# Kernel optimization log

Hardware: AMD Instinct MI355X
Metric: run time of the kernel (lower is better)

Reference implementation:

```python
import jax, jax.numpy as jnp
import numpy as np

B, S, D, H, DFF = 2, 2048, 512, 8, 2048
DK = D // H
EPS = 1e-6  # LayerNormalization eps


def _ln(x, a, b):
    # torch: alpha * (x - mean) / (std + eps) + bias, std is unbiased (ddof=1)
    m = jnp.mean(x, axis=-1, keepdims=True)
    s = jnp.std(x, axis=-1, keepdims=True, ddof=1)
    return a * (x - m) / (s + EPS) + b


def _mha(Q, K, V, mask, Wq, bq, Wk, bk, Wv, bv, Wo, bo):
    Bq, Sq = Q.shape[0], Q.shape[1]
    Sk = K.shape[1]
    q = (Q @ Wq + bq).reshape(Bq, Sq, H, DK).transpose(0, 2, 1, 3)  # bhqd
    k = (K @ Wk + bk).reshape(Bq, Sk, H, DK).transpose(0, 2, 1, 3)  # bhkd
    v = (V @ Wv + bv).reshape(Bq, Sk, H, DK).transpose(0, 2, 1, 3)  # bhkd
    scores = jnp.einsum('bhqd,bhkd->bhqk', q, k) / jnp.sqrt(jnp.float32(DK))
    scores = jnp.where(mask == 0, -jnp.inf, scores)  # masked_fill(mask==0, -inf)
    attn = jax.nn.softmax(scores, axis=-1)  # dropout is identity in eval
    out = jnp.einsum('bhqk,bhkd->bhqd', attn, v)
    out = out.transpose(0, 2, 1, 3).reshape(Bq, Sq, D)
    return out @ Wo + bo


def setup_inputs() -> dict:
    key = jax.random.key(0)
    ks = jax.random.split(key, 20)
    sc = 0.02
    inp = {
        'x': jax.random.normal(ks[0], (B, S, D), jnp.float32),
        'encoder_output': jax.random.normal(ks[1], (B, S, D), jnp.float32),
        'encoder_output_mask': jnp.broadcast_to(jnp.ones((S, S), jnp.int32), (B, 1, S, S)),
        'decoder_mask': jnp.broadcast_to(jnp.tril(jnp.ones((S, S), jnp.int32)), (B, 1, S, S)),
        'sa_Wq': jax.random.normal(ks[2], (D, D), jnp.float32) * sc,
        'sa_bq': jnp.zeros((D,), jnp.float32),
        'sa_Wk': jax.random.normal(ks[3], (D, D), jnp.float32) * sc,
        'sa_bk': jnp.zeros((D,), jnp.float32),
        'sa_Wv': jax.random.normal(ks[4], (D, D), jnp.float32) * sc,
        'sa_bv': jnp.zeros((D,), jnp.float32),
        'sa_Wo': jax.random.normal(ks[5], (D, D), jnp.float32) * sc,
        'sa_bo': jnp.zeros((D,), jnp.float32),
        'ca_Wq': jax.random.normal(ks[6], (D, D), jnp.float32) * sc,
        'ca_bq': jnp.zeros((D,), jnp.float32),
        'ca_Wk': jax.random.normal(ks[7], (D, D), jnp.float32) * sc,
        'ca_bk': jnp.zeros((D,), jnp.float32),
        'ca_Wv': jax.random.normal(ks[8], (D, D), jnp.float32) * sc,
        'ca_bv': jnp.zeros((D,), jnp.float32),
        'ca_Wo': jax.random.normal(ks[9], (D, D), jnp.float32) * sc,
        'ca_bo': jnp.zeros((D,), jnp.float32),
        'ff_W1': jax.random.normal(ks[10], (D, DFF), jnp.float32) * sc,
        'ff_b1': jnp.zeros((DFF,), jnp.float32),
        'ff_W2': jax.random.normal(ks[11], (DFF, D), jnp.float32) * sc,
        'ff_b2': jnp.zeros((D,), jnp.float32),
        'ln0_a': jnp.ones((1,), jnp.float32), 'ln0_b': jnp.zeros((1,), jnp.float32),
        'ln1_a': jnp.ones((1,), jnp.float32), 'ln1_b': jnp.zeros((1,), jnp.float32),
        'ln2_a': jnp.ones((1,), jnp.float32), 'ln2_b': jnp.zeros((1,), jnp.float32),
    }
    return inp


def reference(x, encoder_output, encoder_output_mask, decoder_mask,
              sa_Wq, sa_bq, sa_Wk, sa_bk, sa_Wv, sa_bv, sa_Wo, sa_bo,
              ca_Wq, ca_bq, ca_Wk, ca_bk, ca_Wv, ca_bv, ca_Wo, ca_bo,
              ff_W1, ff_b1, ff_W2, ff_b2,
              ln0_a, ln0_b, ln1_a, ln1_b, ln2_a, ln2_b):
    # Residual 0: pre-norm self-attention (dropout = identity in eval)
    n = _ln(x, ln0_a, ln0_b)
    x = x + _mha(n, n, n, decoder_mask, sa_Wq, sa_bq, sa_Wk, sa_bk, sa_Wv, sa_bv, sa_Wo, sa_bo)
    # Residual 1: pre-norm cross-attention
    n = _ln(x, ln1_a, ln1_b)
    x = x + _mha(n, encoder_output, encoder_output, encoder_output_mask,
                 ca_Wq, ca_bq, ca_Wk, ca_bk, ca_Wv, ca_bv, ca_Wo, ca_bo)
    # Residual 2: pre-norm FFN (Linear -> ReLU -> Linear)
    n = _ln(x, ln2_a, ln2_b)
    x = x + (jax.nn.relu(n @ ff_W1 + ff_b1) @ ff_W2 + ff_b2)
    return x
```

## Files before the change

kernel.cpp:

```cpp
#include <hip/hip_runtime.h>
#include <hip/hip_bf16.h>

typedef __bf16 bf16_t;
typedef __bf16 bf16x8_t __attribute__((ext_vector_type(8)));
typedef float f32x4_t __attribute__((ext_vector_type(4)));

static constexpr int B_ = 2, S_ = 2048, D_ = 512, H_ = 8, DK_ = 64, DFF_ = 2048;
static constexpr int M_ = B_ * S_;
static constexpr float QSCALE = 0.125f * 1.44269504f;

#define VMCNT_BARRIER(N) asm volatile("s_waitcnt vmcnt(" #N ")\n\ts_barrier" ::: "memory")

__device__ __forceinline__ unsigned pkbf(float a, float b) {
  union { bf16_t h; unsigned short u; } x, y;
  x.h = (bf16_t)a; y.h = (bf16_t)b;
  return (unsigned)x.u | ((unsigned)y.u << 16);
}

__device__ __forceinline__ void async16(bf16_t* lds, const bf16_t* g) {
  __builtin_amdgcn_global_load_lds((__attribute__((address_space(1))) void*)g,
                                   (__attribute__((address_space(3))) void*)lds,
                                   16, 0, 0);
}

__global__ __launch_bounds__(256) void ln_kernel(const float* __restrict__ x,
                                                 const float* __restrict__ ga,
                                                 const float* __restrict__ gb,
                                                 bf16_t* __restrict__ out) {
  const int row = blockIdx.x * 4 + (threadIdx.x >> 6);
  const int lane = threadIdx.x & 63;
  const float4* xr = (const float4*)(x + (long)row * D_);
  float4 v0 = xr[lane * 2];
  float4 v1 = xr[lane * 2 + 1];
  float s = v0.x + v0.y + v0.z + v0.w + v1.x + v1.y + v1.z + v1.w;
  float ss = v0.x * v0.x + v0.y * v0.y + v0.z * v0.z + v0.w * v0.w +
             v1.x * v1.x + v1.y * v1.y + v1.z * v1.z + v1.w * v1.w;
#pragma unroll
  for (int m = 1; m < 64; m <<= 1) {
    s += __shfl_xor(s, m);
    ss += __shfl_xor(ss, m);
  }
  const float mean = s * (1.0f / 512.0f);
  float var = (ss - 512.0f * mean * mean) * (1.0f / 511.0f);
  var = fmaxf(var, 0.0f);
  const float sc = ga[0] / (sqrtf(var) + 1e-6f);
  const float sh = gb[0] - mean * sc;
  alignas(16) bf16_t y[8];
  y[0] = (bf16_t)(v0.x * sc + sh);
  y[1] = (bf16_t)(v0.y * sc + sh);
  y[2] = (bf16_t)(v0.z * sc + sh);
  y[3] = (bf16_t)(v0.w * sc + sh);
  y[4] = (bf16_t)(v1.x * sc + sh);
  y[5] = (bf16_t)(v1.y * sc + sh);
  y[6] = (bf16_t)(v1.z * sc + sh);
  y[7] = (bf16_t)(v1.w * sc + sh);
  ((uint4*)(out + (long)row * D_))[lane] = *(uint4*)y;
}

__global__ __launch_bounds__(256) void cvt_bf16(const float* __restrict__ x,
                                                bf16_t* __restrict__ y) {
  const long i = ((long)blockIdx.x * 256 + threadIdx.x) * 8;
  float4 a = *(const float4*)(x + i);
  float4 b = *(const float4*)(x + i + 4);
  alignas(16) bf16_t t[8];
  t[0] = (bf16_t)a.x; t[1] = (bf16_t)a.y; t[2] = (bf16_t)a.z; t[3] = (bf16_t)a.w;
  t[4] = (bf16_t)b.x; t[5] = (bf16_t)b.y; t[6] = (bf16_t)b.z; t[7] = (bf16_t)b.w;
  *(uint4*)(y + i) = *(uint4*)t;
}

__device__ __forceinline__ void wtrans_body(const float* __restrict__ W,
                                            bf16_t* __restrict__ Wt, int K, int N,
                                            int k0, int n0) {
  constexpr int LDT = 65;
  __shared__ float T[64 * LDT];
  const int tid = threadIdx.x;
#pragma unroll
  for (int p = 0; p < 4; ++p) {
    int e = p * 1024 + tid * 4;
    int kr = e >> 6, nc = e & 63;
    float4 f = *(const float4*)(W + (long)(k0 + kr) * N + n0 + nc);
    T[kr * LDT + nc + 0] = f.x;
    T[kr * LDT + nc + 1] = f.y;
    T[kr * LDT + nc + 2] = f.z;
    T[kr * LDT + nc + 3] = f.w;
  }
  __syncthreads();
#pragma unroll
  for (int p = 0; p < 4; ++p) {
    int e = p * 1024 + tid * 4;
    int nr = e >> 6, kc = e & 63;
    alignas(8) bf16_t t[4];
#pragma unroll
    for (int j = 0; j < 4; ++j) t[j] = (bf16_t)T[(kc + j) * LDT + nr];
    *(uint2*)(Wt + (long)(n0 + nr) * K + k0 + kc) = *(uint2*)t;
  }
}

struct WPA { const float* W[10]; bf16_t* T[10]; };
__global__ __launch_bounds__(256) void wprep(WPA a) {
  const int x = blockIdx.x;
  if (x < 512) {
    const int wi = x >> 6, t = x & 63;
    wtrans_body(a.W[wi], a.T[wi], 512, 512, (t >> 3) * 64, (t & 7) * 64);
  } else if (x < 768) {
    const int t = x - 512;
    wtrans_body(a.W[8], a.T[8], 512, 2048, (t & 7) * 64, (t >> 3) * 64);
  } else {
    const int t = x - 768;
    wtrans_body(a.W[9], a.T[9], 2048, 512, (t & 31) * 64, (t >> 5) * 64);
  }
}

__global__ __launch_bounds__(256) void vtrans(const bf16_t* __restrict__ v,
                                              bf16_t* __restrict__ vt) {
  constexpr int LDT = 66;
  __shared__ bf16_t T[64 * LDT];
  const int tid = threadIdx.x;
  const int bh = blockIdx.y, b = bh >> 3, h = bh & 7;
  const int s0 = blockIdx.x * 64;
#pragma unroll
  for (int p = 0; p < 2; ++p) {
    int e = p * 2048 + tid * 8;
    int sr = e >> 6, c = e & 63;
    uint4 u = *(const uint4*)(v + (long)(b * S_ + s0 + sr) * D_ + h * DK_ + c);
    bf16_t* pv = (bf16_t*)&u;
#pragma unroll
    for (int j = 0; j < 8; ++j) T[(c + j) * LDT + sr] = pv[j];
  }
  __syncthreads();
#pragma unroll
  for (int p = 0; p < 2; ++p) {
    int e = p * 2048 + tid * 8;
    int d = e >> 6, sc = e & 63;
    alignas(16) bf16_t t[8];
#pragma unroll
    for (int j = 0; j < 8; ++j) t[j] = T[d * LDT + sc + j];
    *(uint4*)(vt + ((long)bh * DK_ + d) * S_ + s0 + sc) = *(uint4*)t;
  }
}

struct GArg {
  const bf16_t* A;
  const bf16_t* Wt;
  const float* bias;
  const float* res;
  void* out;
  float oscale;
};

template <int MODE>
__global__ __launch_bounds__(256, 2) void gemm_bt(GArg g0, GArg g1, GArg g2,
                                                  int M, int N, int K) {
  __shared__ bf16_t As[3][64 * 64];
  __shared__ bf16_t Bs[3][128 * 64];
  GArg g = (blockIdx.z == 0) ? g0 : (blockIdx.z == 1) ? g1 : g2;
  const int tid = threadIdx.x;
  const int wave = tid >> 6, lane = tid & 63, quad = lane >> 4, l15 = lane & 15;
  const long m0 = (long)blockIdx.x * 64;
  const long n0 = (long)blockIdx.y * 128;
  const int wm = (wave >> 1) * 32;
  const int wn = (wave & 1) * 64;

  const int r8 = lane >> 3;
  const int cg = (lane & 7) ^ r8;
  const bf16_t* Ab = g.A + m0 * (long)K + cg * 8;
  const bf16_t* Bb = g.Wt + n0 * (long)K + cg * 8;

  auto stage = [&](int buf, int k0) {
#pragma unroll
    for (int c = 0; c < 2; ++c) {
      const int row = wave * 16 + c * 8;
      async16(&As[buf][row * 64], Ab + (long)(row + r8) * K + k0);
    }
#pragma unroll
    for (int c = 0; c < 4; ++c) {
      const int row = wave * 32 + c * 8;
      async16(&Bs[buf][row * 64], Bb + (long)(row + r8) * K + k0);
    }
  };

  f32x4_t acc[2][4];
#pragma unroll
  for (int i = 0; i < 2; ++i)
#pragma unroll
    for (int j = 0; j < 4; ++j) acc[i][j] = (f32x4_t){0.f, 0.f, 0.f, 0.f};

  const int KT = K >> 6;
  stage(0, 0);
  stage(1, 64);
  int bc = 0;
  for (int kt = 0; kt < KT; ++kt) {
    if (kt + 1 < KT) { VMCNT_BARRIER(6); } else { VMCNT_BARRIER(0); }
    int bs = bc + 2; if (bs >= 3) bs -= 3;
    if (kt + 2 < KT) stage(bs, (kt + 2) * 64);
    const bf16_t* Al = &As[bc][0];
    const bf16_t* Bl = &Bs[bc][0];
    bf16x8_t af[2][2], bfr[2][4];
#pragma unroll
    for (int ks = 0; ks < 2; ++ks) {
      const int sc = ((ks * 4 + quad) ^ (l15 & 7)) * 8;
#pragma unroll
      for (int i = 0; i < 2; ++i)
        af[ks][i] = *(const bf16x8_t*)&Al[(wm + i * 16 + l15) * 64 + sc];
#pragma unroll
      for (int j = 0; j < 4; ++j)
        bfr[ks][j] = *(const bf16x8_t*)&Bl[(wn + j * 16 + l15) * 64 + sc];
    }
#pragma unroll
    for (int ks = 0; ks < 2; ++ks)
#pragma unroll
      for (int i = 0; i < 2; ++i)
#pragma unroll
        for (int j = 0; j < 4; ++j)
          acc[i][j] = __builtin_amdgcn_mfma_f32_16x16x32_bf16(af[ks][i], bfr[ks][j], acc[i][j], 0, 0, 0);
    bc = (bc + 1 == 3) ? 0 : bc + 1;
  }

#pragma unroll
  for (int i = 0; i < 2; ++i) {
#pragma unroll
    for (int j = 0; j < 4; ++j) {
      const long col = n0 + wn + j * 16 + l15;
      const float bv = g.bias[col];
#pragma unroll
      for (int r = 0; r < 4; ++r) {
        const long row = m0 + wm + i * 16 + quad * 4 + r;
        float v = acc[i][j][r] + bv;
        if constexpr (MODE == 1) v = fmaxf(v, 0.f);
        if constexpr (MODE == 2) {
          ((float*)g.out)[row * N + col] = v + g.res[row * N + col];
        } else {
          ((bf16_t*)g.out)[row * N + col] = (bf16_t)(v * g.oscale);
        }
      }
    }
  }
}

template <bool CAUSAL>
__global__ __launch_bounds__(256, 2) void flash_attn(const bf16_t* __restrict__ Q,
                                                     const bf16_t* __restrict__ Kg,
                                                     const bf16_t* __restrict__ Vt,
                                                     float* __restrict__ po,
                                                     float* __restrict__ pl) {
  __shared__ bf16_t Ks[3][64 * 64];
  __shared__ bf16_t Vs[3][64 * 64];
  __shared__ bf16_t Ps[4][32 * 64];
  const int tid = threadIdx.x, wave = tid >> 6, lane = tid & 63;
  const int quad = lane >> 4, l15 = lane & 15;
  const int bh = blockIdx.y, b = bh >> 3, h = bh & 7;
  const int qt = CAUSAL ? (15 - (int)blockIdx.x) : (int)blockIdx.x;
  const int chunk = blockIdx.z;
  const int ntt = CAUSAL ? (2 * qt + 2) : 32;
  const int n0t = ntt >> 1;
  const int tstart = chunk ? n0t : 0;
  const int tend = chunk ? ntt : n0t;

  const int q0 = qt * 128;
  const int qw = q0 + wave * 32;
  const long base = (long)b * S_ * D_ + (long)h * DK_;
  const long vtbase = (long)bh * DK_ * S_;
  const long prow0 = ((long)(chunk * 16 + bh)) * 2048;

  bf16x8_t qf[2][2];
#pragma unroll
  for (int qh = 0; qh < 2; ++qh)
#pragma unroll
    for (int ks = 0; ks < 2; ++ks)
      qf[qh][ks] = *(const bf16x8_t*)(Q + base + (long)(qw + qh * 16 + l15) * D_ + ks * 32 + quad * 8);

  const int r8 = lane >> 3;
  const int cg8 = (lane & 7) ^ r8;
  const bf16_t* Kb = Kg + base + cg8 * 8;
  const bf16_t* Vb = Vt + vtbase + cg8 * 8;

  auto stage = [&](int buf, int t) {
    const int kk0 = t * 64;
#pragma unroll
    for (int c = 0; c < 2; ++c) {
      const int row = wave * 16 + c * 8;
      async16(&Ks[buf][row * 64], Kb + (long)(kk0 + row + r8) * D_);
      async16(&Vs[buf][row * 64], Vb + (long)(row + r8) * S_ + kk0);
    }
  };

  float li[2] = {0.f, 0.f};
  f32x4_t o[2][4];
#pragma unroll
  for (int qh = 0; qh < 2; ++qh)
#pragma unroll
    for (int db = 0; db < 4; ++db) o[qh][db] = (f32x4_t){0.f, 0.f, 0.f, 0.f};

  bf16_t* Pw = &Ps[wave][0];
  const int pq7 = l15 & 7;

  stage(0, tstart);
  if (tstart + 1 < tend) stage(1, tstart + 1);
  int bc = 0;
  for (int t = tstart; t < tend; ++t) {
    if (t + 1 < tend) { VMCNT_BARRIER(4); } else { VMCNT_BARRIER(0); }
    int bs = bc + 2; if (bs >= 3) bs -= 3;
    if (t + 2 < tend) stage(bs, t + 2);
    const bf16_t* Kt = &Ks[bc][0];
    const bf16_t* Vl = &Vs[bc][0];
    const int kk0 = t * 64;

#pragma unroll
    for (int qh = 0; qh < 2; ++qh) {
      f32x4_t st[4];
#pragma unroll
      for (int nb = 0; nb < 4; ++nb) {
        f32x4_t a = (f32x4_t){0.f, 0.f, 0.f, 0.f};
#pragma unroll
        for (int ks = 0; ks < 2; ++ks) {
          const int scf = ((ks * 4 + quad) ^ (l15 & 7)) * 8;
          const bf16x8_t kf = *(const bf16x8_t*)&Kt[(nb * 16 + l15) * 64 + scf];
          a = __builtin_amdgcn_mfma_f32_16x16x32_bf16(kf, qf[qh][ks], a, 0, 0, 0);
        }
        st[nb] = a;
      }
      const bool domask = CAUSAL && (kk0 + 63 > qw + qh * 16);
#pragma unroll
      for (int nb = 0; nb < 4; ++nb)
#pragma unroll
        for (int r = 0; r < 4; ++r) {
          float v = st[nb][r];
          if (domask && (kk0 + nb * 16 + quad * 4 + r > qw + qh * 16 + l15)) v = -1e30f;
          const float p = exp2f(v);
          st[nb][r] = p;
          li[qh] += p;
        }
      const int prow = (qh * 16 + l15) * 64;
#pragma unroll
      for (int nb = 0; nb < 4; ++nb) {
        uint2 w;
        w.x = pkbf(st[nb][0], st[nb][1]);
        w.y = pkbf(st[nb][2], st[nb][3]);
        const int ck = nb * 2 + (quad >> 1);
        *(uint2*)&Pw[prow + (ck ^ pq7) * 8 + (quad & 1) * 4] = w;
      }
    }

    bf16x8_t pf[2][2];
#pragma unroll
    for (int qh = 0; qh < 2; ++qh)
#pragma unroll
      for (int ks = 0; ks < 2; ++ks)
        pf[qh][ks] = *(const bf16x8_t*)&Pw[(qh * 16 + l15) * 64 + (((ks * 4 + quad) ^ pq7)) * 8];
#pragma unroll
    for (int ks = 0; ks < 2; ++ks) {
#pragma unroll
      for (int db = 0; db < 4; ++db) {
        const int scf = ((ks * 4 + quad) ^ (l15 & 7)) * 8;
        const bf16x8_t vf = *(const bf16x8_t*)&Vl[(db * 16 + l15) * 64 + scf];
#pragma unroll
        for (int qh = 0; qh < 2; ++qh)
          o[qh][db] = __builtin_amdgcn_mfma_f32_16x16x32_bf16(vf, pf[qh][ks], o[qh][db], 0, 0, 0);
      }
    }
    bc = (bc + 1 == 3) ? 0 : bc + 1;
  }

#pragma unroll
  for (int qh = 0; qh < 2; ++qh) {
    li[qh] += __shfl_xor(li[qh], 16);
    li[qh] += __shfl_xor(li[qh], 32);
    const long pr = prow0 + qw + qh * 16 + l15;
#pragma unroll
    for (int db = 0; db < 4; ++db)
      *(f32x4_t*)&po[pr * 64 + db * 16 + quad * 4] = o[qh][db];
    if (quad == 0) pl[pr] = li[qh];
  }
}

__global__ __launch_bounds__(256) void merge_attn(const float* __restrict__ po,
                                                  const float* __restrict__ pl,
                                                  bf16_t* __restrict__ O) {
  const int qt = blockIdx.x, bh = blockIdx.y, b = bh >> 3, h = bh & 7;
  const int t = threadIdx.x;
  const int q = qt * 64 + (t >> 2), d0 = (t & 3) * 16;
  const long r0 = (long)bh * 2048 + q;
  const long r1 = (long)(16 + bh) * 2048 + q;
  const float inv = 1.0f / (pl[r0] + pl[r1]);
  const long i0 = r0 * 64 + d0;
  const long i1 = r1 * 64 + d0;
  alignas(16) bf16_t out[16];
#pragma unroll
  for (int j = 0; j < 4; ++j) {
    f32x4_t a = *(const f32x4_t*)&po[i0 + j * 4];
    f32x4_t c = *(const f32x4_t*)&po[i1 + j * 4];
#pragma unroll
    for (int r = 0; r < 4; ++r) out[j * 4 + r] = (bf16_t)((a[r] + c[r]) * inv);
  }
  const long row = (long)b * S_ + q;
  *(uint4*)(O + row * D_ + h * DK_ + d0) = *(uint4*)&out[0];
  *(uint4*)(O + row * D_ + h * DK_ + d0 + 8) = *(uint4*)&out[8];
}

extern "C" void kernel_launch(void* const* d_in, const int* in_sizes, int n_in,
                              void* d_out, int out_size, void* d_ws, size_t ws_size,
                              hipStream_t stream) {
  const float* x    = (const float*)d_in[0];
  const float* enc  = (const float*)d_in[1];
  const float* saWq = (const float*)d_in[4];  const float* sabq = (const float*)d_in[5];
  const float* saWk = (const float*)d_in[6];  const float* sabk = (const float*)d_in[7];
  const float* saWv = (const float*)d_in[8];  const float* sabv = (const float*)d_in[9];
  const float* saWo = (const float*)d_in[10]; const float* sabo = (const float*)d_in[11];
  const float* caWq = (const float*)d_in[12]; const float* cabq = (const float*)d_in[13];
  const float* caWk = (const float*)d_in[14]; const float* cabk = (const float*)d_in[15];
  const float* caWv = (const float*)d_in[16]; const float* cabv = (const float*)d_in[17];
  const float* caWo = (const float*)d_in[18]; const float* cabo = (const float*)d_in[19];
  const float* ffW1 = (const float*)d_in[20]; const float* ffb1 = (const float*)d_in[21];
  const float* ffW2 = (const float*)d_in[22]; const float* ffb2 = (const float*)d_in[23];
  const float* ln0a = (const float*)d_in[24]; const float* ln0b = (const float*)d_in[25];
  const float* ln1a = (const float*)d_in[26]; const float* ln1b = (const float*)d_in[27];
  const float* ln2a = (const float*)d_in[28]; const float* ln2b = (const float*)d_in[29];

  char* ws = (char*)d_ws;
  size_t off = 0;
  auto alloc = [&](size_t bytes) -> void* {
    void* p = ws + off;
    off += (bytes + 255) & ~(size_t)255;
    return p;
  };
  bf16_t* wt_saq = (bf16_t*)alloc(512 * 512 * 2);
  bf16_t* wt_sak = (bf16_t*)alloc(512 * 512 * 2);
  bf16_t* wt_sav = (bf16_t*)alloc(512 * 512 * 2);
  bf16_t* wt_sao = (bf16_t*)alloc(512 * 512 * 2);
  bf16_t* wt_caq = (bf16_t*)alloc(512 * 512 * 2);
  bf16_t* wt_cak = (bf16_t*)alloc(512 * 512 * 2);
  bf16_t* wt_cav = (bf16_t*)alloc(512 * 512 * 2);
  bf16_t* wt_cao = (bf16_t*)alloc(512 * 512 * 2);
  bf16_t* wt_f1  = (bf16_t*)alloc((size_t)512 * 2048 * 2);
  bf16_t* wt_f2  = (bf16_t*)alloc((size_t)2048 * 512 * 2);
  bf16_t* enc_b  = (bf16_t*)alloc((size_t)M_ * D_ * 2);
  bf16_t* nbuf   = (bf16_t*)alloc((size_t)M_ * D_ * 2);
  bf16_t* qb     = (bf16_t*)alloc((size_t)M_ * D_ * 2);
  bf16_t* kb     = (bf16_t*)alloc((size_t)M_ * D_ * 2);
  bf16_t* vb     = (bf16_t*)alloc((size_t)M_ * D_ * 2);
  bf16_t* vtb    = (bf16_t*)alloc((size_t)M_ * D_ * 2);
  bf16_t* attnb  = (bf16_t*)alloc((size_t)M_ * D_ * 2);
  bf16_t* hid    = (bf16_t*)alloc((size_t)M_ * DFF_ * 2);
  float*  x1     = (float*)alloc((size_t)M_ * D_ * 4);
  float*  x2     = (float*)alloc((size_t)M_ * D_ * 4);
  float*  pl     = (float*)alloc(2 * 16 * 2048 * 4);
  float*  po     = (float*)hid;

  {
    WPA a;
    a.W[0] = saWq; a.T[0] = wt_saq;
    a.W[1] = saWk; a.T[1] = wt_sak;
    a.W[2] = saWv; a.T[2] = wt_sav;
    a.W[3] = saWo; a.T[3] = wt_sao;
    a.W[4] = caWq; a.T[4] = wt_caq;
    a.W[5] = caWk; a.T[5] = wt_cak;
    a.W[6] = caWv; a.T[6] = wt_cav;
    a.W[7] = caWo; a.T[7] = wt_cao;
    a.W[8] = ffW1; a.T[8] = wt_f1;
    a.W[9] = ffW2; a.T[9] = wt_f2;
    wprep<<<1024, 256, 0, stream>>>(a);
  }
  cvt_bf16<<<1024, 256, 0, stream>>>(enc, enc_b);

  ln_kernel<<<1024, 256, 0, stream>>>(x, ln0a, ln0b, nbuf);
  {
    GArg z0{nbuf, wt_saq, sabq, nullptr, qb, QSCALE};
    GArg z1{nbuf, wt_sak, sabk, nullptr, kb, 1.0f};
    GArg z2{nbuf, wt_sav, sabv, nullptr, vb, 1.0f};
    gemm_bt<0><<<dim3(64, 4, 3), 256, 0, stream>>>(z0, z1, z2, M_, 512, 512);
  }
  vtrans<<<dim3(32, 16), 256, 0, stream>>>(vb, vtb);
  flash_attn<true><<<dim3(16, 16, 2), 256, 0, stream>>>(qb, kb, vtb, po, pl);
  merge_attn<<<dim3(32, 16), 256, 0, stream>>>(po, pl, attnb);
  {
    GArg o1{attnb, wt_sao, sabo, x, x1, 1.0f};
    gemm_bt<2><<<dim3(64, 4, 1), 256, 0, stream>>>(o1, o1, o1, M_, 512, 512);
  }

  ln_kernel<<<1024, 256, 0, stream>>>(x1, ln1a, ln1b, nbuf);
  {
    GArg c0{nbuf,  wt_caq, cabq, nullptr, qb, QSCALE};
    GArg c1{enc_b, wt_cak, cabk, nullptr, kb, 1.0f};
    GArg c2{enc_b, wt_cav, cabv, nullptr, vb, 1.0f};
    gemm_bt<0><<<dim3(64, 4, 3), 256, 0, stream>>>(c0, c1, c2, M_, 512, 512);
  }
  vtrans<<<dim3(32, 16), 256, 0, stream>>>(vb, vtb);
  flash_attn<false><<<dim3(16, 16, 2), 256, 0, stream>>>(qb, kb, vtb, po, pl);
  merge_attn<<<dim3(32, 16), 256, 0, stream>>>(po, pl, attnb);
  {
    GArg o2{attnb, wt_cao, cabo, x1, x2, 1.0f};
    gemm_bt<2><<<dim3(64, 4, 1), 256, 0, stream>>>(o2, o2, o2, M_, 512, 512);
  }

  ln_kernel<<<1024, 256, 0, stream>>>(x2, ln2a, ln2b, nbuf);
  {
    GArg f1{nbuf, wt_f1, ffb1, nullptr, hid, 1.0f};
    gemm_bt<1><<<dim3(64, 16, 1), 256, 0, stream>>>(f1, f1, f1, M_, DFF_, 512);
  }
  {
    GArg f2{hid, wt_f2, ffb2, x2, d_out, 1.0f};
    gemm_bt<2><<<dim3(64, 4, 1), 256, 0, stream>>>(f2, f2, f2, M_, 512, DFF_);
  }
}
```

Measured before the change: 385.9 us.

## Fold LayerNorm into GEMM epilogues, merge prep kernels, fuse V transpose, split attention three ways

LayerNorm is applied algebraically inside the projection GEMM epilogues. The GEMMs read an unnormalized bf16 copy of the input and correct with per-row stats and weight column sums, so the separate LN kernels go away. The residual GEMMs emit bf16 copies and accumulate row sum and sum-of-squares with atomics. Weight prep, encoder conversion, stats and column sums are merged into one prep kernel. The V transpose is fused into the QKV GEMM store, the projection GEMMs move to 128x128 tiles with K=32 double buffering, and flash attention is split into three KV chunks. Risks are extra bf16 rounding error from normalizing after the matmul and atomic accumulation order.

```diff
diff --git a/kernel.cpp b/kernel.cpp
--- a/kernel.cpp
+++ b/kernel.cpp
@@ -8,8 +8,6 @@
 static constexpr int B_ = 2, S_ = 2048, D_ = 512, H_ = 8, DK_ = 64, DFF_ = 2048;
 static constexpr int M_ = B_ * S_;
 static constexpr float QSCALE = 0.125f * 1.44269504f;
-
-#define VMCNT_BARRIER(N) asm volatile("s_waitcnt vmcnt(" #N ")\n\ts_barrier" ::: "memory")
 
 __device__ __forceinline__ unsigned pkbf(float a, float b) {
   union { bf16_t h; unsigned short u; } x, y;
@@ -23,137 +21,221 @@
                                    16, 0, 0);
 }
 
-__global__ __launch_bounds__(256) void ln_kernel(const float* __restrict__ x,
-                                                 const float* __restrict__ ga,
-                                                 const float* __restrict__ gb,
-                                                 bf16_t* __restrict__ out) {
-  const int row = blockIdx.x * 4 + (threadIdx.x >> 6);
-  const int lane = threadIdx.x & 63;
-  const float4* xr = (const float4*)(x + (long)row * D_);
-  float4 v0 = xr[lane * 2];
-  float4 v1 = xr[lane * 2 + 1];
-  float s = v0.x + v0.y + v0.z + v0.w + v1.x + v1.y + v1.z + v1.w;
-  float ss = v0.x * v0.x + v0.y * v0.y + v0.z * v0.z + v0.w * v0.w +
-             v1.x * v1.x + v1.y * v1.y + v1.z * v1.z + v1.w * v1.w;
-#pragma unroll
-  for (int m = 1; m < 64; m <<= 1) {
-    s += __shfl_xor(s, m);
-    ss += __shfl_xor(ss, m);
-  }
-  const float mean = s * (1.0f / 512.0f);
-  float var = (ss - 512.0f * mean * mean) * (1.0f / 511.0f);
+struct PrepArg {
+  const float* W[10]; bf16_t* T[10];
+  const float* enc; bf16_t* encb;
+  const float* x; bf16_t* xb; float2* stats0;
+  float* stats12;
+  float* csum[7];
+};
+
+__global__ __launch_bounds__(256) void prep(PrepArg a) {
+  __shared__ float T[64 * 65];
+  const int bx = blockIdx.x, tid = threadIdx.x;
+  if (bx < 1024) {
+    const float* W; bf16_t* Wt; int K, N, k0, n0;
+    if (bx < 512) { int wi = bx >> 6, t = bx & 63; W = a.W[wi]; Wt = a.T[wi]; K = 512; N = 512; k0 = (t >> 3) * 64; n0 = (t & 7) * 64; }
+    else if (bx < 768) { int t = bx - 512; W = a.W[8]; Wt = a.T[8]; K = 512; N = 2048; k0 = (t & 7) * 64; n0 = (t >> 3) * 64; }
+    else { int t = bx - 768; W = a.W[9]; Wt = a.T[9]; K = 2048; N = 512; k0 = (t & 31) * 64; n0 = (t >> 5) * 64; }
+#pragma unroll
+    for (int p = 0; p < 4; ++p) {
+      int e = p * 1024 + tid * 4;
+      int kr = e >> 6, nc = e & 63;
+      float4 f = *(const float4*)(W + (long)(k0 + kr) * N + n0 + nc);
+      T[kr * 65 + nc + 0] = f.x; T[kr * 65 + nc + 1] = f.y;
+      T[kr * 65 + nc + 2] = f.z; T[kr * 65 + nc + 3] = f.w;
+    }
+    __syncthreads();
+#pragma unroll
+    for (int p = 0; p < 4; ++p) {
+      int e = p * 1024 + tid * 4;
+      int nr = e >> 6, kc = e & 63;
+      alignas(8) bf16_t t4[4];
+#pragma unroll
+      for (int j = 0; j < 4; ++j) t4[j] = (bf16_t)T[(kc + j) * 65 + nr];
+      *(uint2*)(Wt + (long)(n0 + nr) * K + k0 + kc) = *(uint2*)t4;
+    }
+  } else if (bx < 2048) {
+    const long i = ((long)(bx - 1024) * 256 + tid) * 8;
+    float4 u = *(const float4*)(a.enc + i);
+    float4 v = *(const float4*)(a.enc + i + 4);
+    alignas(16) bf16_t t[8];
+    t[0] = (bf16_t)u.x; t[1] = (bf16_t)u.y; t[2] = (bf16_t)u.z; t[3] = (bf16_t)u.w;
+    t[4] = (bf16_t)v.x; t[5] = (bf16_t)v.y; t[6] = (bf16_t)v.z; t[7] = (bf16_t)v.w;
+    *(uint4*)(a.encb + i) = *(uint4*)t;
+  } else if (bx < 3072) {
+    const int row = (bx - 2048) * 4 + (tid >> 6);
+    const int lane = tid & 63;
+    const float4* xr = (const float4*)(a.x + (long)row * D_);
+    float4 v0 = xr[lane * 2], v1 = xr[lane * 2 + 1];
+    float s = v0.x + v0.y + v0.z + v0.w + v1.x + v1.y + v1.z + v1.w;
+    float ss = v0.x * v0.x + v0.y * v0.y + v0.z * v0.z + v0.w * v0.w +
+               v1.x * v1.x + v1.y * v1.y + v1.z * v1.z + v1.w * v1.w;
+#pragma unroll
+    for (int m = 1; m < 64; m <<= 1) { s += __shfl_xor(s, m); ss += __shfl_xor(ss, m); }
+    alignas(16) bf16_t y[8];
+    y[0] = (bf16_t)v0.x; y[1] = (bf16_t)v0.y; y[2] = (bf16_t)v0.z; y[3] = (bf16_t)v0.w;
+    y[4] = (bf16_t)v1.x; y[5] = (bf16_t)v1.y; y[6] = (bf16_t)v1.z; y[7] = (bf16_t)v1.w;
+    ((uint4*)(a.xb + (long)row * D_))[lane] = *(uint4*)y;
+    if (lane == 0) a.stats0[row] = make_float2(s, ss);
+  } else if (bx < 3152) {
+    __shared__ float red[256];
+    int b3 = bx - 3072;
+    const float* Wsrc; float* dst; int N, c0;
+    if (b3 < 48) {
+      const int map[6] = {0, 1, 2, 4, 5, 6};
+      int wsel = b3 >> 3;
+      Wsrc = a.W[map[wsel]]; dst = a.csum[wsel]; N = 512; c0 = (b3 & 7) * 64;
+    } else { Wsrc = a.W[8]; dst = a.csum[6]; N = 2048; c0 = (b3 - 48) * 64; }
+    const int col = c0 + (tid & 63);
+    float p = 0.f;
+    for (int k = tid >> 6; k < 512; k += 4) p += Wsrc[(long)k * N + col];
+    red[tid] = p;
+    __syncthreads();
+    if (tid < 64) dst[c0 + tid] = red[tid] + red[tid + 64] + red[tid + 128] + red[tid + 192];
+  } else {
+    const int i = (bx - 3152) * 2048 + tid * 8;
+    *(f32x4_t*)&a.stats12[i] = (f32x4_t){0.f, 0.f, 0.f, 0.f};
+    *(f32x4_t*)&a.stats12[i + 4] = (f32x4_t){0.f, 0.f, 0.f, 0.f};
+  }
+}
+
+__device__ __forceinline__ void ln_coef(float2 st, float ga, float gb,
+                                        float& sc, float& sh) {
+  const float mean = st.x * (1.0f / 512.0f);
+  float var = (st.y - 512.0f * mean * mean) * (1.0f / 511.0f);
   var = fmaxf(var, 0.0f);
-  const float sc = ga[0] / (sqrtf(var) + 1e-6f);
-  const float sh = gb[0] - mean * sc;
-  alignas(16) bf16_t y[8];
-  y[0] = (bf16_t)(v0.x * sc + sh);
-  y[1] = (bf16_t)(v0.y * sc + sh);
-  y[2] = (bf16_t)(v0.z * sc + sh);
-  y[3] = (bf16_t)(v0.w * sc + sh);
-  y[4] = (bf16_t)(v1.x * sc + sh);
-  y[5] = (bf16_t)(v1.y * sc + sh);
-  y[6] = (bf16_t)(v1.z * sc + sh);
-  y[7] = (bf16_t)(v1.w * sc + sh);
-  ((uint4*)(out + (long)row * D_))[lane] = *(uint4*)y;
-}
-
-__global__ __launch_bounds__(256) void cvt_bf16(const float* __restrict__ x,
-                                                bf16_t* __restrict__ y) {
-  const long i = ((long)blockIdx.x * 256 + threadIdx.x) * 8;
-  float4 a = *(const float4*)(x + i);
-  float4 b = *(const float4*)(x + i + 4);
-  alignas(16) bf16_t t[8];
-  t[0] = (bf16_t)a.x; t[1] = (bf16_t)a.y; t[2] = (bf16_t)a.z; t[3] = (bf16_t)a.w;
-  t[4] = (bf16_t)b.x; t[5] = (bf16_t)b.y; t[6] = (bf16_t)b.z; t[7] = (bf16_t)b.w;
-  *(uint4*)(y + i) = *(uint4*)t;
-}
-
-__device__ __forceinline__ void wtrans_body(const float* __restrict__ W,
-                                            bf16_t* __restrict__ Wt, int K, int N,
-                                            int k0, int n0) {
-  constexpr int LDT = 65;
-  __shared__ float T[64 * LDT];
+  sc = ga / (sqrtf(var) + 1e-6f);
+  sh = gb - mean * sc;
+}
+
+struct G128 {
+  const bf16_t* A[3]; const bf16_t* Wt[3];
+  const float* bias[3]; const float* csum[3];
+  void* out[3]; float osc[3];
+  const float2* stats; const float* ga; const float* gb;
+  int N; int zvt;
+};
+
+template <int RELU>
+__global__ __launch_bounds__(256, 2) void gemm128(G128 a) {
+  __shared__ bf16_t As[2][128 * 32];
+  __shared__ bf16_t Bs[2][128 * 32];
+  const int z = blockIdx.z;
+  const bf16_t* A = a.A[z];
+  const bf16_t* Wt = a.Wt[z];
+  const float* bias = a.bias[z];
+  const float* csum = a.csum[z];
+  const int N = a.N;
   const int tid = threadIdx.x;
-#pragma unroll
-  for (int p = 0; p < 4; ++p) {
-    int e = p * 1024 + tid * 4;
-    int kr = e >> 6, nc = e & 63;
-    float4 f = *(const float4*)(W + (long)(k0 + kr) * N + n0 + nc);
-    T[kr * LDT + nc + 0] = f.x;
-    T[kr * LDT + nc + 1] = f.y;
-    T[kr * LDT + nc + 2] = f.z;
-    T[kr * LDT + nc + 3] = f.w;
-  }
-  __syncthreads();
-#pragma unroll
-  for (int p = 0; p < 4; ++p) {
-    int e = p * 1024 + tid * 4;
-    int nr = e >> 6, kc = e & 63;
-    alignas(8) bf16_t t[4];
-#pragma unroll
-    for (int j = 0; j < 4; ++j) t[j] = (bf16_t)T[(kc + j) * LDT + nr];
-    *(uint2*)(Wt + (long)(n0 + nr) * K + k0 + kc) = *(uint2*)t;
-  }
-}
-
-struct WPA { const float* W[10]; bf16_t* T[10]; };
-__global__ __launch_bounds__(256) void wprep(WPA a) {
-  const int x = blockIdx.x;
-  if (x < 512) {
-    const int wi = x >> 6, t = x & 63;
-    wtrans_body(a.W[wi], a.T[wi], 512, 512, (t >> 3) * 64, (t & 7) * 64);
-  } else if (x < 768) {
-    const int t = x - 512;
-    wtrans_body(a.W[8], a.T[8], 512, 2048, (t & 7) * 64, (t >> 3) * 64);
+  const int wave = tid >> 6, lane = tid & 63, quad = lane >> 4, l15 = lane & 15;
+  const long m0 = (long)blockIdx.x * 128;
+  const long n0 = (long)blockIdx.y * 128;
+  const int wm = (wave >> 1) * 64;
+  const int wn = (wave & 1) * 64;
+
+  const int r4 = lane >> 2;
+  const int cg = (lane & 3) ^ ((lane >> 3) & 3);
+  const bf16_t* Ab = A + m0 * 512 + cg * 8;
+  const bf16_t* Bb = Wt + n0 * 512 + cg * 8;
+
+  auto stage = [&](int buf, int k0) {
+#pragma unroll
+    for (int c = 0; c < 2; ++c) {
+      const int row = wave * 32 + c * 16;
+      async16(&As[buf][row * 32], Ab + (long)(row + r4) * 512 + k0);
+      async16(&Bs[buf][row * 32], Bb + (long)(row + r4) * 512 + k0);
+    }
+  };
+
+  f32x4_t acc[4][4];
+#pragma unroll
+  for (int i = 0; i < 4; ++i)
+#pragma unroll
+    for (int j = 0; j < 4; ++j) acc[i][j] = (f32x4_t){0.f, 0.f, 0.f, 0.f};
+
+  const int sc8 = (quad ^ ((l15 >> 1) & 3)) * 8;
+  stage(0, 0);
+  for (int kt = 0; kt < 16; ++kt) {
+    __syncthreads();
+    if (kt + 1 < 16) stage((kt + 1) & 1, (kt + 1) * 32);
+    const bf16_t* Al = &As[kt & 1][0];
+    const bf16_t* Bl = &Bs[kt & 1][0];
+    bf16x8_t af[4], bfr[4];
+#pragma unroll
+    for (int i = 0; i < 4; ++i) af[i] = *(const bf16x8_t*)&Al[(wm + i * 16 + l15) * 32 + sc8];
+#pragma unroll
+    for (int j = 0; j < 4; ++j) bfr[j] = *(const bf16x8_t*)&Bl[(wn + j * 16 + l15) * 32 + sc8];
+#pragma unroll
+    for (int i = 0; i < 4; ++i)
+#pragma unroll
+      for (int j = 0; j < 4; ++j)
+        acc[i][j] = __builtin_amdgcn_mfma_f32_16x16x32_bf16(af[i], bfr[j], acc[i][j], 0, 0, 0);
+  }
+
+  const bool useln = (csum != nullptr);
+  float scr[4][4], shr[4][4];
+  if (useln) {
+    const float gav = a.ga[0], gbv = a.gb[0];
+#pragma unroll
+    for (int i = 0; i < 4; ++i)
+#pragma unroll
+      for (int r = 0; r < 4; ++r) {
+        const int row = (int)m0 + wm + i * 16 + quad * 4 + r;
+        ln_coef(a.stats[row], gav, gbv, scr[i][r], shr[i][r]);
+      }
   } else {
-    const int t = x - 768;
-    wtrans_body(a.W[9], a.T[9], 2048, 512, (t & 31) * 64, (t >> 5) * 64);
-  }
-}
-
-__global__ __launch_bounds__(256) void vtrans(const bf16_t* __restrict__ v,
-                                              bf16_t* __restrict__ vt) {
-  constexpr int LDT = 66;
-  __shared__ bf16_t T[64 * LDT];
-  const int tid = threadIdx.x;
-  const int bh = blockIdx.y, b = bh >> 3, h = bh & 7;
-  const int s0 = blockIdx.x * 64;
-#pragma unroll
-  for (int p = 0; p < 2; ++p) {
-    int e = p * 2048 + tid * 8;
-    int sr = e >> 6, c = e & 63;
-    uint4 u = *(const uint4*)(v + (long)(b * S_ + s0 + sr) * D_ + h * DK_ + c);
-    bf16_t* pv = (bf16_t*)&u;
-#pragma unroll
-    for (int j = 0; j < 8; ++j) T[(c + j) * LDT + sr] = pv[j];
-  }
-  __syncthreads();
-#pragma unroll
-  for (int p = 0; p < 2; ++p) {
-    int e = p * 2048 + tid * 8;
-    int d = e >> 6, sc = e & 63;
-    alignas(16) bf16_t t[8];
-#pragma unroll
-    for (int j = 0; j < 8; ++j) t[j] = T[d * LDT + sc + j];
-    *(uint4*)(vt + ((long)bh * DK_ + d) * S_ + s0 + sc) = *(uint4*)t;
-  }
-}
-
-struct GArg {
-  const bf16_t* A;
-  const bf16_t* Wt;
-  const float* bias;
-  const float* res;
-  void* out;
-  float oscale;
-};
-
-template <int MODE>
-__global__ __launch_bounds__(256, 2) void gemm_bt(GArg g0, GArg g1, GArg g2,
-                                                  int M, int N, int K) {
-  __shared__ bf16_t As[3][64 * 64];
-  __shared__ bf16_t Bs[3][128 * 64];
-  GArg g = (blockIdx.z == 0) ? g0 : (blockIdx.z == 1) ? g1 : g2;
+#pragma unroll
+    for (int i = 0; i < 4; ++i)
+#pragma unroll
+      for (int r = 0; r < 4; ++r) { scr[i][r] = 1.f; shr[i][r] = 0.f; }
+  }
+
+  const bool isVt = (z == a.zvt);
+  const float osc = a.osc[z];
+#pragma unroll
+  for (int i = 0; i < 4; ++i) {
+#pragma unroll
+    for (int j = 0; j < 4; ++j) {
+      const int col = (int)n0 + wn + j * 16 + l15;
+      const float cs = useln ? csum[col] : 0.f;
+      const float bv = bias[col];
+      float v[4];
+#pragma unroll
+      for (int r = 0; r < 4; ++r) {
+        v[r] = scr[i][r] * acc[i][j][r] + shr[i][r] * cs + bv;
+        if constexpr (RELU == 1) v[r] = fmaxf(v[r], 0.f);
+      }
+      if (isVt) {
+        const int row0 = (int)m0 + wm + i * 16 + quad * 4;
+        const int b = row0 >> 11, s = row0 & 2047;
+        const long addr = ((long)(b * 8 + (col >> 6)) * 64 + (col & 63)) * 2048 + s;
+        uint2 w;
+        w.x = pkbf(v[0], v[1]);
+        w.y = pkbf(v[2], v[3]);
+        *(uint2*)((bf16_t*)a.out[z] + addr) = w;
+      } else {
+        bf16_t* outp = (bf16_t*)a.out[z];
+#pragma unroll
+        for (int r = 0; r < 4; ++r) {
+          const long row = m0 + wm + i * 16 + quad * 4 + r;
+          outp[row * N + col] = (bf16_t)(v[r] * osc);
+        }
+      }
+    }
+  }
+}
+
+template <bool STATS>
+__global__ __launch_bounds__(256, 3) void gemm64(const bf16_t* __restrict__ A, int K,
+                                                 const bf16_t* __restrict__ Wt,
+                                                 const float* __restrict__ bias,
+                                                 const float* __restrict__ res,
+                                                 float* __restrict__ out,
+                                                 bf16_t* __restrict__ outb,
+                                                 float* __restrict__ statsOut) {
+  __shared__ bf16_t As[2][64 * 64];
+  __shared__ bf16_t Bs[2][128 * 64];
   const int tid = threadIdx.x;
   const int wave = tid >> 6, lane = tid & 63, quad = lane >> 4, l15 = lane & 15;
   const long m0 = (long)blockIdx.x * 64;
@@ -163,8 +245,8 @@
 
   const int r8 = lane >> 3;
   const int cg = (lane & 7) ^ r8;
-  const bf16_t* Ab = g.A + m0 * (long)K + cg * 8;
-  const bf16_t* Bb = g.Wt + n0 * (long)K + cg * 8;
+  const bf16_t* Ab = A + m0 * (long)K + cg * 8;
+  const bf16_t* Bb = Wt + n0 * (long)K + cg * 8;
 
   auto stage = [&](int buf, int k0) {
 #pragma unroll
@@ -187,64 +269,72 @@
 
   const int KT = K >> 6;
   stage(0, 0);
-  stage(1, 64);
-  int bc = 0;
   for (int kt = 0; kt < KT; ++kt) {
-    if (kt + 1 < KT) { VMCNT_BARRIER(6); } else { VMCNT_BARRIER(0); }
-    int bs = bc + 2; if (bs >= 3) bs -= 3;
-    if (kt + 2 < KT) stage(bs, (kt + 2) * 64);
-    const bf16_t* Al = &As[bc][0];
-    const bf16_t* Bl = &Bs[bc][0];
-    bf16x8_t af[2][2], bfr[2][4];
+    __syncthreads();
+    if (kt + 1 < KT) stage((kt + 1) & 1, (kt + 1) * 64);
+    const bf16_t* Al = &As[kt & 1][0];
+    const bf16_t* Bl = &Bs[kt & 1][0];
 #pragma unroll
     for (int ks = 0; ks < 2; ++ks) {
       const int sc = ((ks * 4 + quad) ^ (l15 & 7)) * 8;
+      bf16x8_t af[2], bfr[4];
+#pragma unroll
+      for (int i = 0; i < 2; ++i) af[i] = *(const bf16x8_t*)&Al[(wm + i * 16 + l15) * 64 + sc];
+#pragma unroll
+      for (int j = 0; j < 4; ++j) bfr[j] = *(const bf16x8_t*)&Bl[(wn + j * 16 + l15) * 64 + sc];
 #pragma unroll
       for (int i = 0; i < 2; ++i)
-        af[ks][i] = *(const bf16x8_t*)&Al[(wm + i * 16 + l15) * 64 + sc];
-#pragma unroll
-      for (int j = 0; j < 4; ++j)
-        bfr[ks][j] = *(const bf16x8_t*)&Bl[(wn + j * 16 + l15) * 64 + sc];
-    }
-#pragma unroll
-    for (int ks = 0; ks < 2; ++ks)
-#pragma unroll
-      for (int i = 0; i < 2; ++i)
 #pragma unroll
         for (int j = 0; j < 4; ++j)
-          acc[i][j] = __builtin_amdgcn_mfma_f32_16x16x32_bf16(af[ks][i], bfr[ks][j], acc[i][j], 0, 0, 0);
-    bc = (bc + 1 == 3) ? 0 : bc + 1;
+          acc[i][j] = __builtin_amdgcn_mfma_f32_16x16x32_bf16(af[i], bfr[j], acc[i][j], 0, 0, 0);
+    }
   }
 
 #pragma unroll
   for (int i = 0; i < 2; ++i) {
+    float rs[4] = {0.f, 0.f, 0.f, 0.f}, rq[4] = {0.f, 0.f, 0.f, 0.f};
 #pragma unroll
     for (int j = 0; j < 4; ++j) {
-      const long col = n0 + wn + j * 16 + l15;
-      const float bv = g.bias[col];
+      const int col = (int)n0 + wn + j * 16 + l15;
+      const float bv = bias[col];
 #pragma unroll
       for (int r = 0; r < 4; ++r) {
         const long row = m0 + wm + i * 16 + quad * 4 + r;
-        float v = acc[i][j][r] + bv;
-        if constexpr (MODE == 1) v = fmaxf(v, 0.f);
-        if constexpr (MODE == 2) {
-          ((float*)g.out)[row * N + col] = v + g.res[row * N + col];
-        } else {
-          ((bf16_t*)g.out)[row * N + col] = (bf16_t)(v * g.oscale);
+        const float v = acc[i][j][r] + bv + res[row * 512 + col];
+        out[row * 512 + col] = v;
+        if constexpr (STATS) {
+          outb[row * 512 + col] = (bf16_t)v;
+          rs[r] += v;
+          rq[r] += v * v;
         }
       }
     }
+    if constexpr (STATS) {
+#pragma unroll
+      for (int r = 0; r < 4; ++r) {
+#pragma unroll
+        for (int m = 1; m < 16; m <<= 1) {
+          rs[r] += __shfl_xor(rs[r], m);
+          rq[r] += __shfl_xor(rq[r], m);
+        }
+        if (l15 == 0) {
+          const long row = m0 + wm + i * 16 + quad * 4 + r;
+          atomicAdd(&statsOut[row * 2], rs[r]);
+          atomicAdd(&statsOut[row * 2 + 1], rq[r]);
+        }
+      }
+    }
   }
 }
 
 template <bool CAUSAL>
-__global__ __launch_bounds__(256, 2) void flash_attn(const bf16_t* __restrict__ Q,
+__global__ __launch_bounds__(256, 3) void flash_attn(const bf16_t* __restrict__ Q,
                                                      const bf16_t* __restrict__ Kg,
                                                      const bf16_t* __restrict__ Vt,
                                                      float* __restrict__ po,
                                                      float* __restrict__ pl) {
-  __shared__ bf16_t Ks[3][64 * 64];
-  __shared__ bf16_t Vs[3][64 * 64];
+  __shared__ bf16_t Ks[2][64 * 64];
+  __shared__ bf16_t Vs[2][64 * 64];
   __shared__ bf16_t Ps[4][32 * 64];
   const int tid = threadIdx.x, wave = tid >> 6, lane = tid & 63;
   const int quad = lane >> 4, l15 = lane & 15;
@@ -252,15 +342,23 @@
   const int qt = CAUSAL ? (15 - (int)blockIdx.x) : (int)blockIdx.x;
   const int chunk = blockIdx.z;
   const int ntt = CAUSAL ? (2 * qt + 2) : 32;
-  const int n0t = ntt >> 1;
-  const int tstart = chunk ? n0t : 0;
-  const int tend = chunk ? ntt : n0t;
-
+  const int tstart = (chunk * ntt) / 3;
+  const int tend = ((chunk + 1) * ntt) / 3;
   const int q0 = qt * 128;
+  const long prow0 = ((long)(chunk * 16 + bh)) * 2048;
+
+  if (tstart >= tend) {
+    const long ob = (prow0 + q0) * 64;
+#pragma unroll
+    for (int p = 0; p < 8; ++p)
+      *(f32x4_t*)&po[ob + (long)tid * 32 + p * 4] = (f32x4_t){0.f, 0.f, 0.f, 0.f};
+    if (tid < 128) pl[prow0 + q0 + tid] = 0.f;
+    return;
+  }
+
   const int qw = q0 + wave * 32;
   const long base = (long)b * S_ * D_ + (long)h * DK_;
   const long vtbase = (long)bh * DK_ * S_;
-  const long prow0 = ((long)(chunk * 16 + bh)) * 2048;
 
   bf16x8_t qf[2][2];
 #pragma unroll
@@ -295,14 +393,12 @@
   const int pq7 = l15 & 7;
 
   stage(0, tstart);
-  if (tstart + 1 < tend) stage(1, tstart + 1);
-  int bc = 0;
   for (int t = tstart; t < tend; ++t) {
-    if (t + 1 < tend) { VMCNT_BARRIER(4); } else { VMCNT_BARRIER(0); }
-    int bs = bc + 2; if (bs >= 3) bs -= 3;
-    if (t + 2 < tend) stage(bs, t + 2);
-    const bf16_t* Kt = &Ks[bc][0];
-    const bf16_t* Vl = &Vs[bc][0];
+    const int buf = (t - tstart) & 1;
+    __syncthreads();
+    if (t + 1 < tend) stage(buf ^ 1, t + 1);
+    const bf16_t* Kt = &Ks[buf][0];
+    const bf16_t* Vl = &Vs[buf][0];
     const int kk0 = t * 64;
 
 #pragma unroll
@@ -346,7 +442,7 @@
     for (int qh = 0; qh < 2; ++qh)
 #pragma unroll
       for (int ks = 0; ks < 2; ++ks)
-        pf[qh][ks] = *(const bf16x8_t*)&Pw[(qh * 16 + l15) * 64 + (((ks * 4 + quad) ^ pq7)) * 8];
+        pf[qh][ks] = *(const bf16x8_t*)&Pw[(qh * 16 + l15) * 64 + ((ks * 4 + quad) ^ pq7) * 8];
 #pragma unroll
     for (int ks = 0; ks < 2; ++ks) {
 #pragma unroll
@@ -358,7 +454,6 @@
           o[qh][db] = __builtin_amdgcn_mfma_f32_16x16x32_bf16(vf, pf[qh][ks], o[qh][db], 0, 0, 0);
       }
     }
-    bc = (bc + 1 == 3) ? 0 : bc + 1;
   }
 
 #pragma unroll
@@ -373,24 +468,24 @@
   }
 }
 
-__global__ __launch_bounds__(256) void merge_attn(const float* __restrict__ po,
-                                                  const float* __restrict__ pl,
-                                                  bf16_t* __restrict__ O) {
+__global__ __launch_bounds__(256) void merge3(const float* __restrict__ po,
+                                              const float* __restrict__ pl,
+                                              bf16_t* __restrict__ O) {
   const int qt = blockIdx.x, bh = blockIdx.y, b = bh >> 3, h = bh & 7;
   const int t = threadIdx.x;
   const int q = qt * 64 + (t >> 2), d0 = (t & 3) * 16;
   const long r0 = (long)bh * 2048 + q;
   const long r1 = (long)(16 + bh) * 2048 + q;
-  const float inv = 1.0f / (pl[r0] + pl[r1]);
-  const long i0 = r0 * 64 + d0;
-  const long i1 = r1 * 64 + d0;
+  const long r2 = (long)(32 + bh) * 2048 + q;
+  const float inv = 1.0f / (pl[r0] + pl[r1] + pl[r2]);
   alignas(16) bf16_t out[16];
 #pragma unroll
   for (int j = 0; j < 4; ++j) {
-    f32x4_t a = *(const f32x4_t*)&po[i0 + j * 4];
-    f32x4_t c = *(const f32x4_t*)&po[i1 + j * 4];
-#pragma unroll
-    for (int r = 0; r < 4; ++r) out[j * 4 + r] = (bf16_t)((a[r] + c[r]) * inv);
+    f32x4_t x0 = *(const f32x4_t*)&po[r0 * 64 + d0 + j * 4];
+    f32x4_t x1 = *(const f32x4_t*)&po[r1 * 64 + d0 + j * 4];
+    f32x4_t x2 = *(const f32x4_t*)&po[r2 * 64 + d0 + j * 4];
+#pragma unroll
+    for (int r = 0; r < 4; ++r) out[j * 4 + r] = (bf16_t)((x0[r] + x1[r] + x2[r]) * inv);
   }
   const long row = (long)b * S_ + q;
   *(uint4*)(O + row * D_ + h * DK_ + d0) = *(uint4*)&out[0];
@@ -434,71 +529,85 @@
   bf16_t* wt_f1  = (bf16_t*)alloc((size_t)512 * 2048 * 2);
   bf16_t* wt_f2  = (bf16_t*)alloc((size_t)2048 * 512 * 2);
   bf16_t* enc_b  = (bf16_t*)alloc((size_t)M_ * D_ * 2);
-  bf16_t* nbuf   = (bf16_t*)alloc((size_t)M_ * D_ * 2);
+  bf16_t* xb     = (bf16_t*)alloc((size_t)M_ * D_ * 2);
   bf16_t* qb     = (bf16_t*)alloc((size_t)M_ * D_ * 2);
   bf16_t* kb     = (bf16_t*)alloc((size_t)M_ * D_ * 2);
-  bf16_t* vb     = (bf16_t*)alloc((size_t)M_ * D_ * 2);
   bf16_t* vtb    = (bf16_t*)alloc((size_t)M_ * D_ * 2);
   bf16_t* attnb  = (bf16_t*)alloc((size_t)M_ * D_ * 2);
   bf16_t* hid    = (bf16_t*)alloc((size_t)M_ * DFF_ * 2);
+  float*  x2     = (float*)alloc((size_t)M_ * D_ * 4);
   float*  x1     = (float*)alloc((size_t)M_ * D_ * 4);
-  float*  x2     = (float*)alloc((size_t)M_ * D_ * 4);
-  float*  pl     = (float*)alloc(2 * 16 * 2048 * 4);
+  bf16_t* x1b    = (bf16_t*)alloc((size_t)M_ * D_ * 2);
+  bf16_t* x2b    = (bf16_t*)alloc((size_t)M_ * D_ * 2);
+  float*  pl     = (float*)alloc(3 * 16 * 2048 * 4);
+  float2* stats0 = (float2*)alloc(4096 * 8);
+  float*  stats12= (float*)alloc(2 * 4096 * 2 * 4);
+  float*  cs_saq = (float*)alloc(512 * 4);
+  float*  cs_sak = (float*)alloc(512 * 4);
+  float*  cs_sav = (float*)alloc(512 * 4);
+  float*  cs_caq = (float*)alloc(512 * 4);
+  float*  cs_cak = (float*)alloc(512 * 4);
+  float*  cs_cav = (float*)alloc(512 * 4);
+  float*  cs_f1  = (float*)alloc(2048 * 4);
   float*  po     = (float*)hid;
+  float*  stats1 = stats12;
+  float*  stats2 = stats12 + 8192;
 
   {
-    WPA a;
-    a.W[0] = saWq; a.T[0] = wt_saq;
-    a.W[1] = saWk; a.T[1] = wt_sak;
-    a.W[2] = saWv; a.T[2] = wt_sav;
-    a.W[3] = saWo; a.T[3] = wt_sao;
-    a.W[4] = caWq; a.T[4] = wt_caq;
-    a.W[5] = caWk; a.T[5] = wt_cak;
-    a.W[6] = caWv; a.T[6] = wt_cav;
-    a.W[7] = caWo; a.T[7] = wt_cao;
-    a.W[8] = ffW1; a.T[8] = wt_f1;
-    a.W[9] = ffW2; a.T[9] = wt_f2;
-    wprep<<<1024, 256, 0, stream>>>(a);
-  }
-  cvt_bf16<<<1024, 256, 0, stream>>>(enc, enc_b);
-
-  ln_kernel<<<1024, 256, 0, stream>>>(x, ln0a, ln0b, nbuf);
+    PrepArg a;
+    a.W[0] = saWq; a.T[0] = wt_saq; a.W[1] = saWk; a.T[1] = wt_sak;
+    a.W[2] = saWv; a.T[2] = wt_sav; a.W[3] = saWo; a.T[3] = wt_sao;
+    a.W[4] = caWq; a.T[4] = wt_caq; a.W[5] = caWk; a.T[5] = wt_cak;
+    a.W[6] = caWv; a.T[6] = wt_cav; a.W[7] = caWo; a.T[7] = wt_cao;
+    a.W[8] = ffW1; a.T[8] = wt_f1;  a.W[9] = ffW2; a.T[9] = wt_f2;
+    a.enc = enc; a.encb = enc_b; a.x = x; a.xb = xb; a.stats0 = stats0;
+    a.stats12 = stats12;
+    a.csum[0] = cs_saq; a.csum[1] = cs_sak; a.csum[2] = cs_sav;
+    a.csum[3] = cs_caq; a.csum[4] = cs_cak; a.csum[5] = cs_cav;
+    a.csum[6] = cs_f1;
+    prep<<<3160, 256, 0, stream>>>(a);
+  }
+
   {
-    GArg z0{nbuf, wt_saq, sabq, nullptr, qb, QSCALE};
-    GArg z1{nbuf, wt_sak, sabk, nullptr, kb, 1.0f};
-    GArg z2{nbuf, wt_sav, sabv, nullptr, vb, 1.0f};
-    gemm_bt<0><<<dim3(64, 4, 3), 256, 0, stream>>>(z0, z1, z2, M_, 512, 512);
-  }
-  vtrans<<<dim3(32, 16), 256, 0, stream>>>(vb, vtb);
-  flash_attn<true><<<dim3(16, 16, 2), 256, 0, stream>>>(qb, kb, vtb, po, pl);
-  merge_attn<<<dim3(32, 16), 256, 0, stream>>>(po, pl, attnb);
+    G128 g;
+    g.A[0] = xb; g.A[1] = xb; g.A[2] = xb;
+    g.Wt[0] = wt_saq; g.Wt[1] = wt_sak; g.Wt[2] = wt_sav;
+    g.bias[0] = sabq; g.bias[1] = sabk; g.bias[2] = sabv;
+    g.csum[0] = cs_saq; g.csum[1] = cs_sak; g.csum[2] = cs_sav;
+    g.out[0] = qb; g.out[1] = kb; g.out[2] = vtb;
+    g.osc[0] = QSCALE; g.osc[1] = 1.f; g.osc[2] = 1.f;
+    g.stats = stats0; g.ga = ln0a; g.gb = ln0b; g.N = 512; g.zvt = 2;
+    gemm128<0><<<dim3(32, 4, 3), 256, 0, stream>>>(g);
+  }
+  flash_attn<true><<<dim3(16, 16, 3), 256, 0, stream>>>(qb, kb, vtb, po, pl);
+  merge3<<<dim3(32, 16), 256, 0, stream>>>(po, pl, attnb);
+  gemm64<true><<<dim3(64, 4), 256, 0, stream>>>(attnb, 512, wt_sao, sabo, x, x1, x1b, stats1);
+
   {
-    GArg o1{attnb, wt_sao, sabo, x, x1, 1.0f};
-    gemm_bt<2><<<dim3(64, 4, 1), 256, 0, stream>>>(o1, o1, o1, M_, 512, 512);
-  }
-
-  ln_kernel<<<1024, 256, 0, stream>>>(x1, ln1a, ln1b, nbuf);
+    G128 g;
+    g.A[0] = x1b; g.A[1] = enc_b; g.A[2] = enc_b;
+    g.Wt[0] = wt_caq; g.Wt[1] = wt_cak; g.Wt[2] = wt_cav;
+    g.bias[0] = cabq; g.bias[1] = cabk; g.bias[2] = cabv;
+    g.csum[0] = cs_caq; g.csum[1] = nullptr; g.csum[2] = nullptr;
+    g.out[0] = qb; g.out[1] = kb; g.out[2] = vtb;
+    g.osc[0] = QSCALE; g.osc[1] = 1.f; g.osc[2] = 1.f;
+    g.stats = (const float2*)stats1; g.ga = ln1a; g.gb = ln1b; g.N = 512; g.zvt = 2;
+    gemm128<0><<<dim3(32, 4, 3), 256, 0, stream>>>(g);
+  }
+  flash_attn<false><<<dim3(16, 16, 3), 256, 0, stream>>>(qb, kb, vtb, po, pl);
+  merge3<<<dim3(32, 16), 256, 0, stream>>>(po, pl, attnb);
+  gemm64<true><<<dim3(64, 4), 256, 0, stream>>>(attnb, 512, wt_cao, cabo, x1, x2, x2b, stats2);
+
   {
-    GArg c0{nbuf,  wt_caq, cabq, nullptr, qb, QSCALE};
-    GArg c1{enc_b, wt_cak, cabk, nullptr, kb, 1.0f};
-    GArg c2{enc_b, wt_cav, cabv, nullptr, vb, 1.0f};
-    gemm_bt<0><<<dim3(64, 4, 3), 256, 0, stream>>>(c0, c1, c2, M_, 512, 512);
-  }
-  vtrans<<<dim3(32, 16), 256, 0, stream>>>(vb, vtb);
-  flash_attn<false><<<dim3(16, 16, 2), 256, 0, stream>>>(qb, kb, vtb, po, pl);
-  merge_attn<<<dim3(32, 16), 256, 0, stream>>>(po, pl, attnb);
-  {
-    GArg o2{attnb, wt_cao, cabo, x1, x2, 1.0f};
-    gemm_bt<2><<<dim3(64, 4, 1), 256, 0, stream>>>(o2, o2, o2, M_, 512, 512);
-  }
-
-  ln_kernel<<<1024, 256, 0, stream>>>(x2, ln2a, ln2b, nbuf);
-  {
-    GArg f1{nbuf, wt_f1, ffb1, nullptr, hid, 1.0f};
-    gemm_bt<1><<<dim3(64, 16, 1), 256, 0, stream>>>(f1, f1, f1, M_, DFF_, 512);
-  }
-  {
-    GArg f2{hid, wt_f2, ffb2, x2, d_out, 1.0f};
-    gemm_bt<2><<<dim3(64, 4, 1), 256, 0, stream>>>(f2, f2, f2, M_, 512, DFF_);
-  }
-}
+    G128 g;
+    g.A[0] = x2b; g.Wt[0] = wt_f1; g.bias[0] = ffb1; g.csum[0] = cs_f1;
+    g.out[0] = hid; g.osc[0] = 1.f;
+    g.A[1] = x2b; g.Wt[1] = wt_f1; g.bias[1] = ffb1; g.csum[1] = cs_f1;
+    g.out[1] = hid; g.osc[1] = 1.f;
+    g.A[2] = x2b; g.Wt[2] = wt_f1; g.bias[2] = ffb1; g.csum[2] = cs_f1;
+    g.out[2] = hid; g.osc[2] = 1.f;
+    g.stats = (const float2*)stats2; g.ga = ln2a; g.gb = ln2b; g.N = 2048; g.zvt = -1;
+    gemm128<1><<<dim3(32, 16, 1), 256, 0, stream>>>(g);
+  }
+  gemm64<false><<<dim3(64, 4), 256, 0, stream>>>(hid, 2048, wt_f2, ffb2, x2, (float*)d_out, nullptr, nullptr);
+}
```

Result: slower. 396.5 us (+2.7%).
